# Performance work log

Measured on AMD Instinct MI355X. Metric: run time of the kernel, lower is better.

## Reference

```python
import jax, jax.numpy as jnp
import numpy as np

NUM_CLUSTERS = 256


def setup_inputs() -> dict:
    key = jax.random.key(0)
    k1, k2, k3 = jax.random.split(key, 3)
    a, b, k = 8192, 8192, NUM_CLUSTERS
    w_mat = jax.random.uniform(k1, (a, b), dtype=jnp.float32)
    # softmax-like assignment probabilities over clusters
    p_l = jax.nn.softmax(jax.random.normal(k2, (a, k), dtype=jnp.float32), axis=-1)
    p_r = jax.nn.softmax(jax.random.normal(k3, (b, k), dtype=jnp.float32), axis=-1)
    clusters_p = jnp.ones((k,), dtype=jnp.float32) / k  # uniform init as in module
    return {"w_mat": w_mat, "p_l": p_l, "p_r": p_r, "clusters_p": clusters_p}


def reference(w_mat, p_l, p_r, clusters_p):
    # Algebraically equivalent to:
    #   ((w[:,:,None] * (p_l[:,None,:] + p_r[None,:,:] - 2*p_l[:,None,:]*p_r[None,:,:]))
    #      .sum((0,1)) / clusters_p).sum()
    # without materializing the (a,b,k) tensor.
    row_w = jnp.sum(w_mat, axis=1)            # (a,)  sum_b w[a,b]
    col_w = jnp.sum(w_mat, axis=0)            # (b,)  sum_a w[a,b]
    rs = row_w @ p_l                           # (k,)  sum_{a,b} w * p_l
    cs = col_w @ p_r                           # (k,)  sum_{a,b} w * p_r
    # cross[k] = sum_{a,b} p_l[a,k] * w[a,b] * p_r[b,k]
    cross = jnp.einsum("ka,ak->k", p_l.T @ w_mat, p_r)  # (k,)
    return jnp.sum((rs + cs - 2.0 * cross) / clusters_p)
```

## Files before the change

### kernel.cpp

```cpp
#include <hip/hip_runtime.h>
#include <stdint.h>

#define A_DIM 8192
#define B_DIM 8192
#define K_CL  256
#define BM    64
#define BK    64
#define NSLAB 4
#define SLABW (B_DIM / NSLAB)
#define NKS   (SLABW / BK)

typedef short bf16x8 __attribute__((ext_vector_type(8)));
typedef float f32x4  __attribute__((ext_vector_type(4)));
typedef float f32x16 __attribute__((ext_vector_type(16)));
typedef unsigned int uint4v __attribute__((ext_vector_type(4)));
typedef unsigned short u16;

__device__ __forceinline__ u16 f2bf(float f) {
    unsigned int u = __float_as_uint(f);
    u += 0x7fffu + ((u >> 16) & 1u);
    return (u16)(u >> 16);
}

__global__ __launch_bounds__(256) void k_prep(const float* __restrict__ pr,
                                              u16* __restrict__ Bpack,
                                              float* __restrict__ out) {
    const int kb2 = blockIdx.x;
    const int t = threadIdx.x;
    if (kb2 == 0 && t == 0) out[0] = 0.0f;
    const int lane = t & 63, wv = t >> 6;
    const int l31 = lane & 31, half = lane >> 5;
#pragma unroll
    for (int ci = 0; ci < 2; ci++) {
        const int c2 = wv * 2 + ci;
        float v[8];
#pragma unroll
        for (int j = 0; j < 8; j++)
            v[j] = pr[(size_t)(kb2 * 16 + half * 8 + j) * K_CL + c2 * 32 + l31];
        union { bf16x8 b; unsigned int u[4]; } o;
#pragma unroll
        for (int j = 0; j < 4; j++)
            o.u[j] = (unsigned int)f2bf(v[2 * j]) | ((unsigned int)f2bf(v[2 * j + 1]) << 16);
        *(bf16x8*)(Bpack + ((size_t)(kb2 * 8 + c2) * 64 + lane) * 8) = o.b;
    }
}

__global__ __launch_bounds__(256, 2) void k_main(const float* __restrict__ w,
                                                 const float* __restrict__ pl,
                                                 const u16* __restrict__ Bpack,
                                                 const float* __restrict__ cp,
                                                 float* __restrict__ out) {
    __shared__ u16 Abf[2][BM * BK];
    __shared__ float rowsum[BM];
    __shared__ float red[4];

    const int bid = blockIdx.x;
    const int slab = bid & 3;
    const int m0 = (bid >> 2) * BM;
    const int tid = threadIdx.x;
    const int lane = tid & 63, wv = tid >> 6;
    const int l31 = lane & 31, half = lane >> 5;
    const int kb2base = slab * 128;

    const int srow = wv * 16 + (lane >> 2);
    const int scg  = lane & 3;
    const float* wthr = w + (size_t)(m0 + srow) * B_DIM + (size_t)slab * SLABW + scg * 16;

    const int wb0 = srow * 128 + ((scg * 32)      ^ ((srow & 7) << 4));
    const int wb1 = srow * 128 + ((scg * 32 + 16) ^ ((srow & 7) << 4));

    float rcp_cp[2];
#pragma unroll
    for (int n2 = 0; n2 < 2; n2++)
        rcp_cp[n2] = 1.0f / cp[wv * 64 + n2 * 32 + l31];

    f32x16 acc[4];
#pragma unroll
    for (int i = 0; i < 4; i++)
#pragma unroll
        for (int r = 0; r < 16; r++) acc[i][r] = 0.f;
    float sums = 0.f;

#define GLOAD(R, ks) do {                                                                \
        const float* gp_ = wthr + (size_t)(ks) * BK;                                     \
        R##0 = *(const f32x4*)(gp_);                                                     \
        R##1 = *(const f32x4*)(gp_ + 4);                                                 \
        R##2 = *(const f32x4*)(gp_ + 8);                                                 \
        R##3 = *(const f32x4*)(gp_ + 12);                                                \
    } while (0)

#define LOADB(arr, ks) do {                                                              \
        _Pragma("unroll")                                                                \
        for (int kf_ = 0; kf_ < 4; kf_++)                                                \
            _Pragma("unroll")                                                            \
            for (int n2_ = 0; n2_ < 2; n2_++)                                            \
                (arr)[kf_ * 2 + n2_] = *(const bf16x8*)(Bpack +                          \
                    (((size_t)(kb2base + (ks) * 4 + kf_) * 8 + wv * 2 + n2_) * 64 + lane) * 8); \
    } while (0)

#define PERM2(hi, lo) __builtin_amdgcn_perm(__float_as_uint(hi), __float_as_uint(lo), 0x07060302u)

#define CONVERT(R, buf) do {                                                             \
        sums += R##0[0]+R##0[1]+R##0[2]+R##0[3] + R##1[0]+R##1[1]+R##1[2]+R##1[3]        \
              + R##2[0]+R##2[1]+R##2[2]+R##2[3] + R##3[0]+R##3[1]+R##3[2]+R##3[3];       \
        uint4v w0_, w1_;                                                                 \
        w0_[0] = PERM2(R##0[1], R##0[0]); w0_[1] = PERM2(R##0[3], R##0[2]);              \
        w0_[2] = PERM2(R##1[1], R##1[0]); w0_[3] = PERM2(R##1[3], R##1[2]);              \
        w1_[0] = PERM2(R##2[1], R##2[0]); w1_[1] = PERM2(R##2[3], R##2[2]);              \
        w1_[2] = PERM2(R##3[1], R##3[0]); w1_[3] = PERM2(R##3[3], R##3[2]);              \
        *(uint4v*)((char*)&Abf[(buf)][0] + wb0) = w0_;                                   \
        *(uint4v*)((char*)&Abf[(buf)][0] + wb1) = w1_;                                   \
    } while (0)

#define COMPUTE(cur, arr) do {                                                           \
        const char* ab_ = (const char*)&Abf[(cur)][0];                                   \
        const int sx_ = (l31 & 7) << 4;                                                  \
        _Pragma("unroll")                                                                \
        for (int kf_ = 0; kf_ < 4; kf_++) {                                              \
            bf16x8 a0_ = *(const bf16x8*)(ab_ + (l31 * 128        + ((kf_ * 32 + half * 16) ^ sx_))); \
            bf16x8 a1_ = *(const bf16x8*)(ab_ + ((32 + l31) * 128 + ((kf_ * 32 + half * 16) ^ sx_))); \
            acc[0] = __builtin_amdgcn_mfma_f32_32x32x16_bf16(a0_, (arr)[kf_ * 2 + 0], acc[0], 0, 0, 0); \
            acc[1] = __builtin_amdgcn_mfma_f32_32x32x16_bf16(a0_, (arr)[kf_ * 2 + 1], acc[1], 0, 0, 0); \
            acc[2] = __builtin_amdgcn_mfma_f32_32x32x16_bf16(a1_, (arr)[kf_ * 2 + 0], acc[2], 0, 0, 0); \
            acc[3] = __builtin_amdgcn_mfma_f32_32x32x16_bf16(a1_, (arr)[kf_ * 2 + 1], acc[3], 0, 0, 0); \
        }                                                                                \
    } while (0)

#define BODYX(ks, WAITN, BC, BN, RC, RN, DOB, DOG, DOCONV, DOBAR) do {                   \
        if (DOB) LOADB(BN, (ks) + 1);                                                    \
        if (DOG) GLOAD(RN, (ks) + 2);                                                    \
        asm volatile("s_waitcnt vmcnt(" #WAITN ")" ::: "memory");                        \
        __builtin_amdgcn_sched_barrier(0);                                               \
        if (DOCONV) CONVERT(RC, ((ks) + 1) & 1);                                         \
        COMPUTE((ks) & 1, BC);                                                           \
        if (DOBAR) {                                                                     \
            asm volatile("s_waitcnt lgkmcnt(0)" ::: "memory");                           \
            __builtin_amdgcn_s_barrier();                                                \
            __builtin_amdgcn_sched_barrier(0);                                           \
        }                                                                                \
    } while (0)

    f32x4 rA0, rA1, rA2, rA3, rB0, rB1, rB2, rB3;
    bf16x8 bA[8], bB[8];

    GLOAD(rA, 0);
    LOADB(bA, 0);
    GLOAD(rB, 1);
    asm volatile("s_waitcnt vmcnt(12)" ::: "memory");
    __builtin_amdgcn_sched_barrier(0);
    CONVERT(rA, 0);
    asm volatile("s_waitcnt lgkmcnt(0)" ::: "memory");
    __builtin_amdgcn_s_barrier();
    __builtin_amdgcn_sched_barrier(0);

    for (int ks = 0; ks < NKS - 2; ks += 2) {
        BODYX(ks,     12, bA, bB, rB, rA, 1, 1, 1, 1);
        BODYX(ks + 1, 12, bB, bA, rA, rB, 1, 1, 1, 1);
    }
    BODYX(30, 8, bA, bB, rB, rA, 1, 0, 1, 1);
    BODYX(31, 0, bB, bA, rA, rB, 0, 0, 0, 0);

#undef BODYX
#undef COMPUTE
#undef CONVERT
#undef PERM2
#undef LOADB
#undef GLOAD

    {
        float v = sums;
        v += __shfl_xor(v, 1, 64);
        v += __shfl_xor(v, 2, 64);
        if ((lane & 3) == 0) rowsum[srow] = v;
    }
    __syncthreads();

    float tot = 0.f;
#pragma unroll
    for (int mf = 0; mf < 2; mf++) {
#pragma unroll
        for (int reg = 0; reg < 16; reg++) {
            const int lrow = mf * 32 + (reg & 3) + 8 * (reg >> 2) + 4 * half;
            const float rs = rowsum[lrow];
            const float* plrow = pl + (size_t)(m0 + lrow) * K_CL + wv * 64 + l31;
#pragma unroll
            for (int n2 = 0; n2 < 2; n2++) {
                const float q = acc[mf * 2 + n2][reg];
                const float p = plrow[n2 * 32];
                tot += (q + p * (rs - 2.0f * q)) * rcp_cp[n2];
            }
        }
    }
    for (int o = 32; o; o >>= 1) tot += __shfl_down(tot, o, 64);
    if (lane == 0) red[wv] = tot;
    __syncthreads();
    if (tid == 0) atomicAdd(out, red[0] + red[1] + red[2] + red[3]);
}

extern "C" void kernel_launch(void* const* d_in, const int* in_sizes, int n_in,
                              void* d_out, int out_size, void* d_ws, size_t ws_size,
                              hipStream_t stream) {
    const float* w  = (const float*)d_in[0];
    const float* pl = (const float*)d_in[1];
    const float* pr = (const float*)d_in[2];
    const float* cp = (const float*)d_in[3];
    float* out = (float*)d_out;

    u16* Bpack = (u16*)d_ws;

    k_prep<<<dim3(512), dim3(256), 0, stream>>>(pr, Bpack, out);
    k_main<<<dim3(128 * NSLAB), dim3(256), 0, stream>>>(w, pl, Bpack, cp, out);
}
```

Before: 72.28 us.

## Give each wave a private 32-row tile spanning all 256 clusters, removing block barriers

Restructures the main kernel so each wave owns 32 rows and computes all 256 cluster columns, with 8 accumulators instead of 4. Each wave stages its own rows through a private LDS buffer, so the per-step block-wide barrier is gone. The B-operand load is pipelined per kf step, and MFMA priority is raised with setprio. The K dimension is split across 8 slabs instead of 4, and the grid and row-sum reduction change to match. The cost is more register pressure from the accumulators and more B-operand traffic per wave, since each wave now reads all 256 columns of p_r.

```diff
diff --git a/kernel.cpp b/kernel.cpp
--- a/kernel.cpp
+++ b/kernel.cpp
@@ -4,16 +4,13 @@
 #define A_DIM 8192
 #define B_DIM 8192
 #define K_CL  256
-#define BM    64
-#define BK    64
-#define NSLAB 4
+#define NSLAB 8
 #define SLABW (B_DIM / NSLAB)
-#define NKS   (SLABW / BK)
+#define NKS   (SLABW / 64)
 
 typedef short bf16x8 __attribute__((ext_vector_type(8)));
 typedef float f32x4  __attribute__((ext_vector_type(4)));
 typedef float f32x16 __attribute__((ext_vector_type(16)));
-typedef unsigned int uint4v __attribute__((ext_vector_type(4)));
 typedef unsigned short u16;
 
 __device__ __forceinline__ u16 f2bf(float f) {
@@ -50,151 +47,144 @@
                                                  const u16* __restrict__ Bpack,
                                                  const float* __restrict__ cp,
                                                  float* __restrict__ out) {
-    __shared__ u16 Abf[2][BM * BK];
-    __shared__ float rowsum[BM];
+    __shared__ u16 Abf[4][2][2048];
+    __shared__ float rowsum_s[4][32];
     __shared__ float red[4];
 
     const int bid = blockIdx.x;
-    const int slab = bid & 3;
-    const int m0 = (bid >> 2) * BM;
+    const int slab = bid & 7;
+    const int mt  = bid >> 3;
     const int tid = threadIdx.x;
     const int lane = tid & 63, wv = tid >> 6;
     const int l31 = lane & 31, half = lane >> 5;
-    const int kb2base = slab * 128;
-
-    const int srow = wv * 16 + (lane >> 2);
-    const int scg  = lane & 3;
-    const float* wthr = w + (size_t)(m0 + srow) * B_DIM + (size_t)slab * SLABW + scg * 16;
-
-    const int wb0 = srow * 128 + ((scg * 32)      ^ ((srow & 7) << 4));
-    const int wb1 = srow * 128 + ((scg * 32 + 16) ^ ((srow & 7) << 4));
-
-    float rcp_cp[2];
-#pragma unroll
-    for (int n2 = 0; n2 < 2; n2++)
-        rcp_cp[n2] = 1.0f / cp[wv * 64 + n2 * 32 + l31];
-
-    f32x16 acc[4];
-#pragma unroll
-    for (int i = 0; i < 4; i++)
+    const int g4 = lane >> 4, c16 = lane & 15;
+
+    const int m0w = mt * 128 + wv * 32;
+    const size_t kbase = (size_t)slab * SLABW;
+    const int kb2base = slab * 64;
+
+    const float* wthr = w + (size_t)(m0w + g4) * B_DIM + kbase + c16 * 4;
+    u16* lds = &Abf[wv][0][0];
+    const int swz = (l31 & 7) << 4;
+
+    f32x16 acc[8];
+#pragma unroll
+    for (int i = 0; i < 8; i++)
 #pragma unroll
         for (int r = 0; r < 16; r++) acc[i][r] = 0.f;
-    float sums = 0.f;
-
-#define GLOAD(R, ks) do {                                                                \
-        const float* gp_ = wthr + (size_t)(ks) * BK;                                     \
-        R##0 = *(const f32x4*)(gp_);                                                     \
-        R##1 = *(const f32x4*)(gp_ + 4);                                                 \
-        R##2 = *(const f32x4*)(gp_ + 8);                                                 \
-        R##3 = *(const f32x4*)(gp_ + 12);                                                \
-    } while (0)
-
-#define LOADB(arr, ks) do {                                                              \
-        _Pragma("unroll")                                                                \
-        for (int kf_ = 0; kf_ < 4; kf_++)                                                \
-            _Pragma("unroll")                                                            \
-            for (int n2_ = 0; n2_ < 2; n2_++)                                            \
-                (arr)[kf_ * 2 + n2_] = *(const bf16x8*)(Bpack +                          \
-                    (((size_t)(kb2base + (ks) * 4 + kf_) * 8 + wv * 2 + n2_) * 64 + lane) * 8); \
+    float sm[8] = {0.f, 0.f, 0.f, 0.f, 0.f, 0.f, 0.f, 0.f};
+
+    f32x4 G[8];
+    bf16x8 Bc[8], Bn[8];
+
+#define WAIT8 do { asm volatile("s_waitcnt vmcnt(8)" ::: "memory"); __builtin_amdgcn_sched_barrier(0); } while (0)
+#define WAIT0 do { asm volatile("s_waitcnt vmcnt(0)" ::: "memory"); __builtin_amdgcn_sched_barrier(0); } while (0)
+#define LGKM0 do { asm volatile("s_waitcnt lgkmcnt(0)" ::: "memory"); __builtin_amdgcn_sched_barrier(0); } while (0)
+
+#define GLOAD(ks) do {                                                                   \
+        _Pragma("unroll")                                                                \
+        for (int j_ = 0; j_ < 8; j_++)                                                   \
+            G[j_] = *(const f32x4*)(wthr + (size_t)(4 * j_) * B_DIM + (size_t)(ks) * 64);\
+    } while (0)
+
+#define LOADB(arr, s_, kf_) do {                                                         \
+        const u16* bp_ = Bpack + (size_t)(kb2base + (s_) * 4 + (kf_)) * 512 + lane * 8;  \
+        _Pragma("unroll")                                                                \
+        for (int n2_ = 0; n2_ < 8; n2_++)                                                \
+            (arr)[n2_] = *(const bf16x8*)(bp_ + n2_ * 512);                              \
     } while (0)
 
 #define PERM2(hi, lo) __builtin_amdgcn_perm(__float_as_uint(hi), __float_as_uint(lo), 0x07060302u)
 
-#define CONVERT(R, buf) do {                                                             \
-        sums += R##0[0]+R##0[1]+R##0[2]+R##0[3] + R##1[0]+R##1[1]+R##1[2]+R##1[3]        \
-              + R##2[0]+R##2[1]+R##2[2]+R##2[3] + R##3[0]+R##3[1]+R##3[2]+R##3[3];       \
-        uint4v w0_, w1_;                                                                 \
-        w0_[0] = PERM2(R##0[1], R##0[0]); w0_[1] = PERM2(R##0[3], R##0[2]);              \
-        w0_[2] = PERM2(R##1[1], R##1[0]); w0_[3] = PERM2(R##1[3], R##1[2]);              \
-        w1_[0] = PERM2(R##2[1], R##2[0]); w1_[1] = PERM2(R##2[3], R##2[2]);              \
-        w1_[2] = PERM2(R##3[1], R##3[0]); w1_[3] = PERM2(R##3[3], R##3[2]);              \
-        *(uint4v*)((char*)&Abf[(buf)][0] + wb0) = w0_;                                   \
-        *(uint4v*)((char*)&Abf[(buf)][0] + wb1) = w1_;                                   \
-    } while (0)
-
-#define COMPUTE(cur, arr) do {                                                           \
-        const char* ab_ = (const char*)&Abf[(cur)][0];                                   \
-        const int sx_ = (l31 & 7) << 4;                                                  \
-        _Pragma("unroll")                                                                \
-        for (int kf_ = 0; kf_ < 4; kf_++) {                                              \
-            bf16x8 a0_ = *(const bf16x8*)(ab_ + (l31 * 128        + ((kf_ * 32 + half * 16) ^ sx_))); \
-            bf16x8 a1_ = *(const bf16x8*)(ab_ + ((32 + l31) * 128 + ((kf_ * 32 + half * 16) ^ sx_))); \
-            acc[0] = __builtin_amdgcn_mfma_f32_32x32x16_bf16(a0_, (arr)[kf_ * 2 + 0], acc[0], 0, 0, 0); \
-            acc[1] = __builtin_amdgcn_mfma_f32_32x32x16_bf16(a0_, (arr)[kf_ * 2 + 1], acc[1], 0, 0, 0); \
-            acc[2] = __builtin_amdgcn_mfma_f32_32x32x16_bf16(a1_, (arr)[kf_ * 2 + 0], acc[2], 0, 0, 0); \
-            acc[3] = __builtin_amdgcn_mfma_f32_32x32x16_bf16(a1_, (arr)[kf_ * 2 + 1], acc[3], 0, 0, 0); \
+#define CONVERT(bufsel) do {                                                             \
+        char* lb_ = (char*)lds + (bufsel) * 4096;                                        \
+        _Pragma("unroll")                                                                \
+        for (int j_ = 0; j_ < 8; j_++) {                                                 \
+            sm[j_] += G[j_][0] + G[j_][1] + G[j_][2] + G[j_][3];                         \
+            uint2 pj_;                                                                   \
+            pj_.x = PERM2(G[j_][1], G[j_][0]);                                           \
+            pj_.y = PERM2(G[j_][3], G[j_][2]);                                           \
+            *(uint2*)(lb_ + (512 * j_ + 128 * g4)                                        \
+                          + ((c16 * 8) ^ (g4 << 4) ^ ((j_ & 1) << 6))) = pj_;            \
         }                                                                                \
     } while (0)
 
-#define BODYX(ks, WAITN, BC, BN, RC, RN, DOB, DOG, DOCONV, DOBAR) do {                   \
-        if (DOB) LOADB(BN, (ks) + 1);                                                    \
-        if (DOG) GLOAD(RN, (ks) + 2);                                                    \
-        asm volatile("s_waitcnt vmcnt(" #WAITN ")" ::: "memory");                        \
-        __builtin_amdgcn_sched_barrier(0);                                               \
-        if (DOCONV) CONVERT(RC, ((ks) + 1) & 1);                                         \
-        COMPUTE((ks) & 1, BC);                                                           \
-        if (DOBAR) {                                                                     \
-            asm volatile("s_waitcnt lgkmcnt(0)" ::: "memory");                           \
-            __builtin_amdgcn_s_barrier();                                                \
-            __builtin_amdgcn_sched_barrier(0);                                           \
-        }                                                                                \
-    } while (0)
-
-    f32x4 rA0, rA1, rA2, rA3, rB0, rB1, rB2, rB3;
-    bf16x8 bA[8], bB[8];
-
-    GLOAD(rA, 0);
-    LOADB(bA, 0);
-    GLOAD(rB, 1);
-    asm volatile("s_waitcnt vmcnt(12)" ::: "memory");
-    __builtin_amdgcn_sched_barrier(0);
-    CONVERT(rA, 0);
-    asm volatile("s_waitcnt lgkmcnt(0)" ::: "memory");
-    __builtin_amdgcn_s_barrier();
-    __builtin_amdgcn_sched_barrier(0);
-
-    for (int ks = 0; ks < NKS - 2; ks += 2) {
-        BODYX(ks,     12, bA, bB, rB, rA, 1, 1, 1, 1);
-        BODYX(ks + 1, 12, bB, bA, rA, rB, 1, 1, 1, 1);
-    }
-    BODYX(30, 8, bA, bB, rB, rA, 1, 0, 1, 1);
-    BODYX(31, 0, bB, bA, rA, rB, 0, 0, 0, 0);
-
-#undef BODYX
-#undef COMPUTE
+#define KFSTEP(kf_, bufsel, Barr) do {                                                   \
+        bf16x8 a_ = *(const bf16x8*)((const char*)lds + (bufsel) * 4096 + l31 * 128      \
+                                     + (((kf_) * 32 + half * 16) ^ swz));                \
+        __builtin_amdgcn_s_setprio(1);                                                   \
+        _Pragma("unroll")                                                                \
+        for (int n2_ = 0; n2_ < 8; n2_++)                                                \
+            acc[n2_] = __builtin_amdgcn_mfma_f32_32x32x16_bf16(a_, (Barr)[n2_],          \
+                                                               acc[n2_], 0, 0, 0);       \
+        __builtin_amdgcn_s_setprio(0);                                                   \
+    } while (0)
+
+    GLOAD(0);
+    WAIT0;
+    CONVERT(0);
+    GLOAD(1);
+    LOADB(Bc, 0, 0);
+    LGKM0;
+
+    for (int s = 0; s < NKS - 1; ++s) {
+        const int buf = s & 1;
+        LOADB(Bn, s, 1);      WAIT8; KFSTEP(0, buf, Bc);
+        LOADB(Bc, s, 2);      WAIT8; KFSTEP(1, buf, Bn);
+        LOADB(Bn, s, 3);      WAIT8; KFSTEP(2, buf, Bc);
+        LOADB(Bc, s + 1, 0);  WAIT8; KFSTEP(3, buf, Bn);
+        CONVERT(buf ^ 1);
+        if (s < NKS - 2) GLOAD(s + 2);
+        LGKM0;
+    }
+    LOADB(Bn, 15, 1); WAIT8; KFSTEP(0, 1, Bc);
+    LOADB(Bc, 15, 2); WAIT8; KFSTEP(1, 1, Bn);
+    LOADB(Bn, 15, 3); WAIT8; KFSTEP(2, 1, Bc);
+    WAIT0;                   KFSTEP(3, 1, Bn);
+
+#undef KFSTEP
 #undef CONVERT
 #undef PERM2
 #undef LOADB
 #undef GLOAD
 
     {
-        float v = sums;
-        v += __shfl_xor(v, 1, 64);
-        v += __shfl_xor(v, 2, 64);
-        if ((lane & 3) == 0) rowsum[srow] = v;
-    }
-    __syncthreads();
+#pragma unroll
+        for (int j = 0; j < 8; j++) {
+            float v = sm[j];
+            v += __shfl_xor(v, 1, 64);
+            v += __shfl_xor(v, 2, 64);
+            v += __shfl_xor(v, 4, 64);
+            v += __shfl_xor(v, 8, 64);
+            if (c16 == 0) rowsum_s[wv][4 * j + g4] = v;
+        }
+    }
+    float rcp_cp[8];
+#pragma unroll
+    for (int n2 = 0; n2 < 8; n2++)
+        rcp_cp[n2] = 1.0f / cp[n2 * 32 + l31];
 
     float tot = 0.f;
 #pragma unroll
-    for (int mf = 0; mf < 2; mf++) {
-#pragma unroll
-        for (int reg = 0; reg < 16; reg++) {
-            const int lrow = mf * 32 + (reg & 3) + 8 * (reg >> 2) + 4 * half;
-            const float rs = rowsum[lrow];
-            const float* plrow = pl + (size_t)(m0 + lrow) * K_CL + wv * 64 + l31;
-#pragma unroll
-            for (int n2 = 0; n2 < 2; n2++) {
-                const float q = acc[mf * 2 + n2][reg];
-                const float p = plrow[n2 * 32];
-                tot += (q + p * (rs - 2.0f * q)) * rcp_cp[n2];
-            }
+    for (int reg = 0; reg < 16; reg++) {
+        const int lrow = (reg & 3) + 8 * (reg >> 2) + 4 * half;
+        const float rs = rowsum_s[wv][lrow];
+        const float* plrow = pl + (size_t)(m0w + lrow) * K_CL + l31;
+#pragma unroll
+        for (int n2 = 0; n2 < 8; n2++) {
+            const float q = acc[n2][reg];
+            const float p = plrow[n2 * 32];
+            tot += (q + p * (rs - 2.0f * q)) * rcp_cp[n2];
         }
     }
     for (int o = 32; o; o >>= 1) tot += __shfl_down(tot, o, 64);
     if (lane == 0) red[wv] = tot;
     __syncthreads();
     if (tid == 0) atomicAdd(out, red[0] + red[1] + red[2] + red[3]);
+
+#undef WAIT8
+#undef WAIT0
+#undef LGKM0
 }
 
 extern "C" void kernel_launch(void* const* d_in, const int* in_sizes, int n_in,
@@ -209,5 +199,5 @@
     u16* Bpack = (u16*)d_ws;
 
     k_prep<<<dim3(512), dim3(256), 0, stream>>>(pr, Bpack, out);
-    k_main<<<dim3(128 * NSLAB), dim3(256), 0, stream>>>(w, pl, Bpack, cp, out);
-}
+    k_main<<<dim3(64 * NSLAB), dim3(256), 0, stream>>>(w, pl, Bpack, cp, out);
+}
```

After: 68.22 us. 5.6% less time.
